# Performance work log

Hardware: AMD Instinct MI355X
Metric: run time of the kernel (lower is better)

## Reference

```python
import jax, jax.numpy as jnp
import numpy as np

N_NODES = 50000
N_EDGES = 800000
HID = 64
N_LAYERS = 3
N_CLASSES = 5
N_GRAPHS = 64
BN_EPS = 1e-5


def setup_inputs() -> dict:
    key = jax.random.key(0)
    ks = jax.random.split(key, 24)
    inp = {}
    inp["x"] = jax.random.normal(ks[0], (N_NODES, 5), dtype=jnp.float32)
    inp["edge_attr"] = jax.random.normal(ks[1], (N_EDGES, 5), dtype=jnp.float32)
    inp["edge_index"] = jax.random.randint(ks[2], (2, N_EDGES), 0, N_NODES, dtype=jnp.int32)
    inp["batch"] = jnp.sort(jax.random.randint(ks[3], (N_NODES,), 0, N_GRAPHS, dtype=jnp.int32))
    s = 0.1
    inp["node_W"] = jax.random.normal(ks[4], (5, HID), dtype=jnp.float32) * s
    inp["node_b"] = jnp.zeros((HID,), jnp.float32)
    inp["edge_W"] = jax.random.normal(ks[5], (5, HID), dtype=jnp.float32) * s
    inp["edge_b"] = jnp.zeros((HID,), jnp.float32)
    # per-layer params stacked on leading dim of size N_LAYERS
    inp["lin_W"] = jax.random.normal(ks[6], (N_LAYERS, HID, HID), dtype=jnp.float32) * s
    inp["lin_b"] = jnp.zeros((N_LAYERS, HID), jnp.float32)
    inp["mlp_W1"] = jax.random.normal(ks[7], (N_LAYERS, HID, HID), dtype=jnp.float32) * s
    inp["mlp_b1"] = jnp.zeros((N_LAYERS, HID), jnp.float32)
    inp["mlp_W2"] = jax.random.normal(ks[8], (N_LAYERS, HID, HID), dtype=jnp.float32) * s
    inp["mlp_b2"] = jnp.zeros((N_LAYERS, HID), jnp.float32)
    inp["bn_g"] = jnp.ones((N_LAYERS, HID), jnp.float32)
    inp["bn_b"] = jnp.zeros((N_LAYERS, HID), jnp.float32)
    inp["head_W1"] = jax.random.normal(ks[9], (HID * 3, HID), dtype=jnp.float32) * s
    inp["head_b1"] = jnp.zeros((HID,), jnp.float32)
    inp["head_W2"] = jax.random.normal(ks[10], (HID, N_CLASSES), dtype=jnp.float32) * s
    inp["head_b2"] = jnp.zeros((N_CLASSES,), jnp.float32)
    return inp


def _forward(x, edge_attr, edge_index, batch, node_W, node_b, edge_W, edge_b,
             lin_W, lin_b, mlp_W1, mlp_b1, mlp_W2, mlp_b2, bn_g, bn_b,
             head_W1, head_b1, head_W2, head_b2):
    h = x @ node_W + node_b                      # [N, H]
    e = edge_attr @ edge_W + edge_b              # [E, H]
    src, dst = edge_index[0], edge_index[1]
    n = h.shape[0]
    inv_std = 1.0 / jnp.sqrt(1.0 + BN_EPS)       # BN eval: running mean=0, var=1
    for l in range(N_LAYERS):
        # GINEConv: m = relu(x_src + Lin(edge_attr)); aggregate sum at dst; eps=0
        m = jax.nn.relu(h[src] + e @ lin_W[l] + lin_b[l])   # [E, H]
        agg = jax.ops.segment_sum(m, dst, num_segments=n)    # [N, H]
        z = h + agg
        z = jax.nn.relu(z @ mlp_W1[l] + mlp_b1[l]) @ mlp_W2[l] + mlp_b2[l]
        z = bn_g[l] * (z * inv_std) + bn_b[l]
        h = jax.nn.relu(z)
    # pooling over graphs
    counts = jax.ops.segment_sum(jnp.ones((n,), h.dtype), batch, num_segments=N_GRAPHS)
    h_sum = jax.ops.segment_sum(h, batch, num_segments=N_GRAPHS)
    h_mean = h_sum / jnp.maximum(counts, 1.0)[:, None]
    h_max = jax.ops.segment_max(h, batch, num_segments=N_GRAPHS)
    h_max = jnp.where(counts[:, None] > 0, h_max, 0.0)
    hc = jnp.concatenate([h_mean, h_max, h_sum], axis=-1)    # [G, 3H]
    return jax.nn.relu(hc @ head_W1 + head_b1) @ head_W2 + head_b2


def reference(x, edge_attr, edge_index, batch, node_W, node_b, edge_W, edge_b,
              lin_W, lin_b, mlp_W1, mlp_b1, mlp_W2, mlp_b2, bn_g, bn_b,
              head_W1, head_b1, head_W2, head_b2):
    return _forward(x, edge_attr, edge_index, batch, node_W, node_b, edge_W, edge_b,
                    lin_W, lin_b, mlp_W1, mlp_b1, mlp_W2, mlp_b2, bn_g, bn_b,
                    head_W1, head_b1, head_W2, head_b2)
```

## Files before the change

kernel.cpp:

```cpp
#include <hip/hip_runtime.h>
#include <hip/hip_bf16.h>

#define HID 64
#define N_LAYERS 3
#define N_GRAPHS 64
#define N_CLASSES 5

__global__ __launch_bounds__(256) void node_embed_kernel(
    const float* __restrict__ x, const float* __restrict__ W,
    const float* __restrict__ b, float* __restrict__ h, int N)
{
    int tid = blockIdx.x * 256 + threadIdx.x;
    int n = tid >> 6;
    int c = tid & 63;
    if (n >= N) return;
    const float* xr = x + (size_t)n * 5;
    float acc = b[c];
#pragma unroll
    for (int k = 0; k < 5; ++k) acc = fmaf(xr[k], W[k * 64 + c], acc);
    h[(size_t)n * 64 + c] = acc;
}

__global__ __launch_bounds__(384) void combine_weights_kernel(
    const float* __restrict__ edge_W, const float* __restrict__ edge_b,
    const float* __restrict__ lin_W, const float* __restrict__ lin_b,
    float* __restrict__ Wc, float* __restrict__ bc)
{
    int l = blockIdx.x;
    int c = threadIdx.x & 63;
    int k = threadIdx.x >> 6;
    const float* LW = lin_W + (size_t)l * 64 * 64;
    if (k < 5) {
        float acc = 0.f;
        for (int j = 0; j < 64; ++j) acc = fmaf(edge_W[k * 64 + j], LW[j * 64 + c], acc);
        Wc[l * 320 + k * 64 + c] = acc;
    } else {
        float acc = lin_b[l * 64 + c];
        for (int j = 0; j < 64; ++j) acc = fmaf(edge_b[j], LW[j * 64 + c], acc);
        bc[l * 64 + c] = acc;
    }
}

__global__ __launch_bounds__(256) void hist_kernel(
    const int* __restrict__ ei, int* __restrict__ deg, int E)
{
    int e = blockIdx.x * 256 + threadIdx.x;
    if (e < E) atomicAdd(&deg[ei[E + e]], 1);
}

__global__ __launch_bounds__(256) void scan1_kernel(
    const int* __restrict__ deg, int* __restrict__ bsum, int N)
{
    __shared__ int s[256];
    int t = threadIdx.x;
    int i = blockIdx.x * 256 + t;
    int v = (i < N) ? deg[i] : 0;
    s[t] = v; __syncthreads();
    for (int off = 128; off > 0; off >>= 1) {
        if (t < off) s[t] += s[t + off];
        __syncthreads();
    }
    if (t == 0) bsum[blockIdx.x] = s[0];
}

__global__ __launch_bounds__(256) void scan2_kernel(
    const int* __restrict__ bsum, int* __restrict__ bpre, int NBLK)
{
    __shared__ int s[256];
    int t = threadIdx.x;
    int v = (t < NBLK) ? bsum[t] : 0;
    s[t] = v; __syncthreads();
    for (int off = 1; off < 256; off <<= 1) {
        int x = (t >= off) ? s[t - off] : 0;
        __syncthreads();
        s[t] += x;
        __syncthreads();
    }
    if (t < NBLK) bpre[t] = s[t] - v;
}

__global__ __launch_bounds__(256) void scan3_kernel(
    const int* __restrict__ deg, const int* __restrict__ bpre,
    int* __restrict__ rowptr, int N, int E)
{
    __shared__ int s[256];
    int t = threadIdx.x;
    int i = blockIdx.x * 256 + t;
    int v = (i < N) ? deg[i] : 0;
    s[t] = v; __syncthreads();
    for (int off = 1; off < 256; off <<= 1) {
        int x = (t >= off) ? s[t - off] : 0;
        __syncthreads();
        s[t] += x;
        __syncthreads();
    }
    if (i < N) rowptr[i] = bpre[blockIdx.x] + s[t] - v;
    if (i == N - 1) rowptr[N] = E;
}

__global__ __launch_bounds__(256) void scatter_kernel(
    const int* __restrict__ ei, const float* __restrict__ ea,
    int* __restrict__ cursor, float* __restrict__ packed,
    int* __restrict__ csrc, int E)
{
    int e = blockIdx.x * 256 + threadIdx.x;
    if (e >= E) return;
    int src = ei[e];
    int dst = ei[E + e];
    int pos = atomicAdd(&cursor[dst], 1);
    const float* p = ea + (size_t)e * 5;
    float4 r0 = make_float4(p[0], p[1], p[2], p[3]);
    float4 r1 = make_float4(p[4], 0.f, 0.f, 0.f);
    float4* q = reinterpret_cast<float4*>(packed + (size_t)pos * 8);
    q[0] = r0;
    q[1] = r1;
    csrc[pos] = src;
}

__global__ __launch_bounds__(256) void agg_kernel(
    const int* __restrict__ rowptr, const int* __restrict__ csrc,
    const float* __restrict__ packed,
    const float* __restrict__ h, const float* __restrict__ Wc,
    const float* __restrict__ bc, float* __restrict__ agg, int N)
{
    int lane = threadIdx.x & 63;
    float w0 = Wc[0 * 64 + lane];
    float w1 = Wc[1 * 64 + lane];
    float w2 = Wc[2 * 64 + lane];
    float w3 = Wc[3 * 64 + lane];
    float w4 = Wc[4 * 64 + lane];
    float bb = bc[lane];

    int wid = (blockIdx.x * 256 + threadIdx.x) >> 6;
    int nw  = (gridDim.x * 256) >> 6;
    for (int n = wid; n < N; n += nw) {
        int eb = rowptr[n];
        int ee = rowptr[n + 1];
        float acc = 0.f;
        for (int base = eb; base < ee; base += 64) {
            int cnt = min(64, ee - base);
            int sv = csrc[base + min(lane, cnt - 1)];
            int j = 0;
            for (; j + 3 < cnt; j += 4) {
                int s0 = __shfl(sv, j + 0);
                int s1 = __shfl(sv, j + 1);
                int s2 = __shfl(sv, j + 2);
                int s3 = __shfl(sv, j + 3);
                float h0 = h[(size_t)s0 * 64 + lane];
                float h1 = h[(size_t)s1 * 64 + lane];
                float h2 = h[(size_t)s2 * 64 + lane];
                float h3 = h[(size_t)s3 * 64 + lane];
                const float4* q = reinterpret_cast<const float4*>(packed + (size_t)(base + j) * 8);
                float4 r0a = q[0], r0b = q[1];
                float4 r1a = q[2], r1b = q[3];
                float4 r2a = q[4], r2b = q[5];
                float4 r3a = q[6], r3b = q[7];
                float m0 = bb + h0;
                m0 = fmaf(r0a.x, w0, m0); m0 = fmaf(r0a.y, w1, m0);
                m0 = fmaf(r0a.z, w2, m0); m0 = fmaf(r0a.w, w3, m0);
                m0 = fmaf(r0b.x, w4, m0);
                float m1 = bb + h1;
                m1 = fmaf(r1a.x, w0, m1); m1 = fmaf(r1a.y, w1, m1);
                m1 = fmaf(r1a.z, w2, m1); m1 = fmaf(r1a.w, w3, m1);
                m1 = fmaf(r1b.x, w4, m1);
                float m2 = bb + h2;
                m2 = fmaf(r2a.x, w0, m2); m2 = fmaf(r2a.y, w1, m2);
                m2 = fmaf(r2a.z, w2, m2); m2 = fmaf(r2a.w, w3, m2);
                m2 = fmaf(r2b.x, w4, m2);
                float m3 = bb + h3;
                m3 = fmaf(r3a.x, w0, m3); m3 = fmaf(r3a.y, w1, m3);
                m3 = fmaf(r3a.z, w2, m3); m3 = fmaf(r3a.w, w3, m3);
                m3 = fmaf(r3b.x, w4, m3);
                acc += fmaxf(m0, 0.f);
                acc += fmaxf(m1, 0.f);
                acc += fmaxf(m2, 0.f);
                acc += fmaxf(m3, 0.f);
            }
            for (; j < cnt; ++j) {
                int s0 = __shfl(sv, j);
                float h0 = h[(size_t)s0 * 64 + lane];
                const float4* q = reinterpret_cast<const float4*>(packed + (size_t)(base + j) * 8);
                float4 r0 = q[0];
                float4 r1 = q[1];
                float m = bb + h0;
                m = fmaf(r0.x, w0, m);
                m = fmaf(r0.y, w1, m);
                m = fmaf(r0.z, w2, m);
                m = fmaf(r0.w, w3, m);
                m = fmaf(r1.x, w4, m);
                acc += fmaxf(m, 0.f);
            }
        }
        agg[(size_t)n * 64 + lane] = acc;
    }
}

__global__ __launch_bounds__(256) void edge_kernel(
    const int* __restrict__ ei, const float* __restrict__ ea,
    const float* __restrict__ h, const float* __restrict__ Wc,
    const float* __restrict__ bc, float* __restrict__ agg, int E)
{
    int lane = threadIdx.x & 63;
    float w0 = Wc[0 * 64 + lane];
    float w1 = Wc[1 * 64 + lane];
    float w2 = Wc[2 * 64 + lane];
    float w3 = Wc[3 * 64 + lane];
    float w4 = Wc[4 * 64 + lane];
    float bb = bc[lane];

    int wave   = (blockIdx.x * 256 + threadIdx.x) >> 6;
    int nwaves = (gridDim.x * 256) >> 6;
    for (int e = wave; e < E; e += nwaves) {
        int src = ei[e];
        int dst = ei[E + e];
        const float* eap = ea + (size_t)e * 5;
        float m = bb + h[(size_t)src * 64 + lane];
        m = fmaf(eap[0], w0, m);
        m = fmaf(eap[1], w1, m);
        m = fmaf(eap[2], w2, m);
        m = fmaf(eap[3], w3, m);
        m = fmaf(eap[4], w4, m);
        m = fmaxf(m, 0.f);
        atomicAdd(&agg[(size_t)dst * 64 + lane], m);
    }
}

__global__ __launch_bounds__(256) void node_mlp_kernel(
    const float* __restrict__ h, const float* __restrict__ agg,
    const float* __restrict__ W1, const float* __restrict__ b1v,
    const float* __restrict__ W2, const float* __restrict__ b2v,
    const float* __restrict__ bng, const float* __restrict__ bnb,
    float* __restrict__ hout, int N)
{
    __shared__ float zbuf[4][64];
    int lane = threadIdx.x & 63;
    int w = threadIdx.x >> 6;

    float w1c[64], w2c[64];
#pragma unroll
    for (int k = 0; k < 64; ++k) w1c[k] = W1[k * 64 + lane];
#pragma unroll
    for (int k = 0; k < 64; ++k) w2c[k] = W2[k * 64 + lane];

    const float inv_std = 0.99999500003749981f;
    float bias1 = b1v[lane];
    float bias2 = b2v[lane];
    float scale = bng[lane] * inv_std;
    float shift = bnb[lane];

    int wid = blockIdx.x * 4 + w;
    int nw  = gridDim.x * 4;
    for (int n = wid; n < N; n += nw) {
        size_t off = (size_t)n * 64 + lane;
        float z = h[off] + agg[off];
        zbuf[w][lane] = z;
        float acc = bias1;
#pragma unroll
        for (int k4 = 0; k4 < 16; ++k4) {
            float4 zk = *reinterpret_cast<const float4*>(&zbuf[w][k4 * 4]);
            acc = fmaf(zk.x, w1c[k4 * 4 + 0], acc);
            acc = fmaf(zk.y, w1c[k4 * 4 + 1], acc);
            acc = fmaf(zk.z, w1c[k4 * 4 + 2], acc);
            acc = fmaf(zk.w, w1c[k4 * 4 + 3], acc);
        }
        float t = fmaxf(acc, 0.f);
        zbuf[w][lane] = t;
        float acc2 = bias2;
#pragma unroll
        for (int k4 = 0; k4 < 16; ++k4) {
            float4 tk = *reinterpret_cast<const float4*>(&zbuf[w][k4 * 4]);
            acc2 = fmaf(tk.x, w2c[k4 * 4 + 0], acc2);
            acc2 = fmaf(tk.y, w2c[k4 * 4 + 1], acc2);
            acc2 = fmaf(tk.z, w2c[k4 * 4 + 2], acc2);
            acc2 = fmaf(tk.w, w2c[k4 * 4 + 3], acc2);
        }
        float y = fmaf(acc2, scale, shift);
        hout[off] = fmaxf(y, 0.f);
    }
}

__global__ __launch_bounds__(256) void pool_kernel(
    const float* __restrict__ h, const int* __restrict__ batch,
    float* __restrict__ psum, int* __restrict__ pmaxi, int* __restrict__ pcount, int N)
{
    int lane = threadIdx.x & 63;
    int chunks = gridDim.x * 4;
    int wid = blockIdx.x * 4 + (threadIdx.x >> 6);
    int CH = (N + chunks - 1) / chunks;
    int n0 = wid * CH;
    int n1 = min(N, n0 + CH);
    if (n0 >= n1) return;

    int gcur = batch[n0];
    float s = 0.f, mx = 0.f;
    int cnt = 0;
    for (int n = n0; n < n1; ++n) {
        int g = batch[n];
        if (g != gcur) {
            atomicAdd(&psum[gcur * 64 + lane], s);
            atomicMax(&pmaxi[gcur * 64 + lane], __float_as_int(mx));
            if (lane == 0) atomicAdd(&pcount[gcur], cnt);
            gcur = g; s = 0.f; mx = 0.f; cnt = 0;
        }
        float v = h[(size_t)n * 64 + lane];
        s += v;
        mx = fmaxf(mx, v);
        ++cnt;
    }
    atomicAdd(&psum[gcur * 64 + lane], s);
    atomicMax(&pmaxi[gcur * 64 + lane], __float_as_int(mx));
    if (lane == 0) atomicAdd(&pcount[gcur], cnt);
}

__global__ __launch_bounds__(256) void head_kernel(
    const float* __restrict__ psum, const int* __restrict__ pmaxi,
    const int* __restrict__ pcount,
    const float* __restrict__ W1, const float* __restrict__ b1,
    const float* __restrict__ W2, const float* __restrict__ b2,
    float* __restrict__ out)
{
    __shared__ float hc[192];
    __shared__ float part[4][64];
    __shared__ float tbuf[64];
    int g = blockIdx.x;
    int tid = threadIdx.x;
    int lane = tid & 63;
    int w = tid >> 6;

    if (tid < 192) {
        int sec = tid >> 6;
        int c = tid & 63;
        float s = psum[g * 64 + c];
        float v;
        if (sec == 0) {
            int cn = pcount[g];
            v = s / fmaxf((float)cn, 1.f);
        } else if (sec == 1) {
            v = __int_as_float(pmaxi[g * 64 + c]);
        } else {
            v = s;
        }
        hc[sec * 64 + c] = v;
    }
    __syncthreads();

    float acc = (w == 0) ? b1[lane] : 0.f;
#pragma unroll
    for (int kk = 0; kk < 48; ++kk) {
        int k = w * 48 + kk;
        acc = fmaf(hc[k], W1[k * 64 + lane], acc);
    }
    part[w][lane] = acc;
    __syncthreads();

    if (w == 0) {
        float t = part[0][lane] + part[1][lane] + part[2][lane] + part[3][lane];
        t = fmaxf(t, 0.f);
        tbuf[lane] = t;
        if (lane < N_CLASSES) {
            float o = b2[lane];
            for (int j = 0; j < 64; ++j) o = fmaf(tbuf[j], W2[j * N_CLASSES + lane], o);
            out[g * N_CLASSES + lane] = o;
        }
    }
}

extern "C" void kernel_launch(void* const* d_in, const int* in_sizes, int n_in,
                              void* d_out, int out_size, void* d_ws, size_t ws_size,
                              hipStream_t stream)
{
    const float* x         = (const float*)d_in[0];
    const float* edge_attr = (const float*)d_in[1];
    const int*   edge_index= (const int*)  d_in[2];
    const int*   batch     = (const int*)  d_in[3];
    const float* node_W    = (const float*)d_in[4];
    const float* node_b    = (const float*)d_in[5];
    const float* edge_W    = (const float*)d_in[6];
    const float* edge_b    = (const float*)d_in[7];
    const float* lin_W     = (const float*)d_in[8];
    const float* lin_b     = (const float*)d_in[9];
    const float* mlp_W1    = (const float*)d_in[10];
    const float* mlp_b1    = (const float*)d_in[11];
    const float* mlp_W2    = (const float*)d_in[12];
    const float* mlp_b2    = (const float*)d_in[13];
    const float* bn_g      = (const float*)d_in[14];
    const float* bn_b      = (const float*)d_in[15];
    const float* head_W1   = (const float*)d_in[16];
    const float* head_b1   = (const float*)d_in[17];
    const float* head_W2   = (const float*)d_in[18];
    const float* head_b2   = (const float*)d_in[19];
    float* out = (float*)d_out;

    const int N = in_sizes[0] / 5;
    const int E = in_sizes[1] / 5;
    const int NBLK = (N + 255) / 256;
    const size_t HB = (size_t)N * HID * sizeof(float);
    const size_t PB = (size_t)E * 8 * sizeof(float);
    const size_t SB = ((size_t)E * sizeof(int) + 1023) & ~(size_t)1023;

    char* ws = (char*)d_ws;
    float* h    = (float*)(ws);
    float* agg  = (float*)(ws + HB);
    const size_t NEEDED = 2 * HB + PB + SB + (size_t)(1 << 20);
    const bool use_csr = (ws_size >= NEEDED);

    char* meta = use_csr ? (ws + 2 * HB + PB + SB) : (ws + 2 * HB);
    float* packed = (float*)(ws + 2 * HB);
    int*   csrc   = (int*)  (ws + 2 * HB + PB);
    int*   rowptr = (int*)(meta);
    int*   cursor = (int*)(meta + 200 * 1024);
    int*   deg    = (int*)(meta + 400 * 1024);
    int*   bsum   = (int*)(meta + 600 * 1024);
    int*   bpre   = (int*)(meta + 601 * 1024);
    float* Wc     = (float*)(meta + 608 * 1024);
    float* bc     = (float*)(meta + 616 * 1024);
    float* psum   = (float*)(meta + 620 * 1024);
    int*   pmaxi  = (int*)(meta + 636 * 1024);
    int*   pcnt   = (int*)(meta + 652 * 1024);

    node_embed_kernel<<<(N * HID + 255) / 256, 256, 0, stream>>>(x, node_W, node_b, h, N);
    combine_weights_kernel<<<N_LAYERS, 384, 0, stream>>>(edge_W, edge_b, lin_W, lin_b, Wc, bc);

    if (use_csr) {
        hipMemsetAsync(deg, 0, (size_t)N * sizeof(int), stream);
        hist_kernel<<<(E + 255) / 256, 256, 0, stream>>>(edge_index, deg, E);
        scan1_kernel<<<NBLK, 256, 0, stream>>>(deg, bsum, N);
        scan2_kernel<<<1, 256, 0, stream>>>(bsum, bpre, NBLK);
        scan3_kernel<<<NBLK, 256, 0, stream>>>(deg, bpre, rowptr, N, E);
        hipMemcpyAsync(cursor, rowptr, (size_t)N * sizeof(int),
                       hipMemcpyDeviceToDevice, stream);
        scatter_kernel<<<(E + 255) / 256, 256, 0, stream>>>(edge_index, edge_attr,
                                                            cursor, packed, csrc, E);
    }

    for (int l = 0; l < N_LAYERS; ++l) {
        if (use_csr) {
            agg_kernel<<<2048, 256, 0, stream>>>(rowptr, csrc, packed, h,
                                                 Wc + l * 320, bc + l * 64, agg, N);
        } else {
            hipMemsetAsync(agg, 0, HB, stream);
            edge_kernel<<<2048, 256, 0, stream>>>(edge_index, edge_attr, h,
                                                  Wc + l * 320, bc + l * 64, agg, E);
        }
        node_mlp_kernel<<<768, 256, 0, stream>>>(h, agg,
                                                 mlp_W1 + (size_t)l * HID * HID, mlp_b1 + l * HID,
                                                 mlp_W2 + (size_t)l * HID * HID, mlp_b2 + l * HID,
                                                 bn_g + l * HID, bn_b + l * HID, h, N);
    }

    hipMemsetAsync(psum, 0, (636 - 620) * 1024 + 16384 + 256, stream);
    pool_kernel<<<196, 256, 0, stream>>>(h, batch, psum, pmaxi, pcnt, N);
    head_kernel<<<N_GRAPHS, 256, 0, stream>>>(psum, pmaxi, pcnt,
                                              head_W1, head_b1, head_W2, head_b2, out);
}
```

Baseline: 444.9 us.

## Build CSR via two-level bucket partition and per-bucket local sort

Replaces the per-node histogram, three-pass scan and global-atomic scatter with a bucket sort. Edges are first grouped into 256-node buckets, staged through shared memory so each chunk writes contiguous runs, then each bucket is sorted locally in shared memory to produce rowptr, csrc and the packed edge attributes. The aim is to cut global atomic contention and random scattered writes during CSR construction. The cost is an extra pass over a temporary record buffer that aliases the h/agg region, plus binary searches in the flush loop. Edge order within a node is no longer deterministic.

```diff
diff --git a/kernel.cpp b/kernel.cpp
--- a/kernel.cpp
+++ b/kernel.cpp
@@ -5,6 +5,8 @@
 #define N_LAYERS 3
 #define N_GRAPHS 64
 #define N_CLASSES 5
+#define CHUNK 4096
+#define MAXB 1024
 
 __global__ __launch_bounds__(256) void node_embed_kernel(
     const float* __restrict__ x, const float* __restrict__ W,
@@ -41,80 +43,142 @@
     }
 }
 
-__global__ __launch_bounds__(256) void hist_kernel(
-    const int* __restrict__ ei, int* __restrict__ deg, int E)
-{
-    int e = blockIdx.x * 256 + threadIdx.x;
-    if (e < E) atomicAdd(&deg[ei[E + e]], 1);
-}
-
-__global__ __launch_bounds__(256) void scan1_kernel(
-    const int* __restrict__ deg, int* __restrict__ bsum, int N)
-{
-    __shared__ int s[256];
+
+__global__ __launch_bounds__(256) void bucket_hist_kernel(
+    const int* __restrict__ ei, int* __restrict__ bhist, int E, int nb)
+{
+    __shared__ int lh[MAXB];
+    for (int i = threadIdx.x; i < nb; i += 256) lh[i] = 0;
+    __syncthreads();
+    int stride = gridDim.x * 256;
+    for (int e = blockIdx.x * 256 + threadIdx.x; e < E; e += stride)
+        atomicAdd(&lh[ei[E + e] >> 8], 1);
+    __syncthreads();
+    for (int i = threadIdx.x; i < nb; i += 256)
+        if (lh[i]) atomicAdd(&bhist[i], lh[i]);
+}
+
+__global__ __launch_bounds__(1024) void bucket_scan_kernel(
+    const int* __restrict__ bhist, int* __restrict__ boff, int* __restrict__ bcur,
+    int nb, int E)
+{
+    __shared__ int s[MAXB];
     int t = threadIdx.x;
-    int i = blockIdx.x * 256 + t;
-    int v = (i < N) ? deg[i] : 0;
+    int v = (t < nb) ? bhist[t] : 0;
     s[t] = v; __syncthreads();
-    for (int off = 128; off > 0; off >>= 1) {
-        if (t < off) s[t] += s[t + off];
-        __syncthreads();
-    }
-    if (t == 0) bsum[blockIdx.x] = s[0];
-}
-
-__global__ __launch_bounds__(256) void scan2_kernel(
-    const int* __restrict__ bsum, int* __restrict__ bpre, int NBLK)
-{
-    __shared__ int s[256];
-    int t = threadIdx.x;
-    int v = (t < NBLK) ? bsum[t] : 0;
-    s[t] = v; __syncthreads();
-    for (int off = 1; off < 256; off <<= 1) {
+    for (int off = 1; off < MAXB; off <<= 1) {
         int x = (t >= off) ? s[t - off] : 0;
         __syncthreads();
         s[t] += x;
         __syncthreads();
     }
-    if (t < NBLK) bpre[t] = s[t] - v;
-}
-
-__global__ __launch_bounds__(256) void scan3_kernel(
-    const int* __restrict__ deg, const int* __restrict__ bpre,
-    int* __restrict__ rowptr, int N, int E)
-{
-    __shared__ int s[256];
+    if (t < nb) { int ex = s[t] - v; boff[t] = ex; bcur[t] = ex; }
+    if (t == 0) boff[nb] = E;
+}
+
+__global__ __launch_bounds__(1024) void partition_kernel(
+    const int* __restrict__ ei, const float* __restrict__ ea,
+    int* __restrict__ bcur, float* __restrict__ tmprec, int E, int nb)
+{
+    __shared__ float stage[CHUNK * 8];
+    __shared__ int ihist[MAXB];
+    __shared__ int iscan[MAXB];
+    __shared__ int cnt2[MAXB];
+    __shared__ int gbase[MAXB];
     int t = threadIdx.x;
-    int i = blockIdx.x * 256 + t;
-    int v = (i < N) ? deg[i] : 0;
-    s[t] = v; __syncthreads();
+    int e0 = blockIdx.x * CHUNK;
+    int cnt = min(CHUNK, E - e0);
+
+    ihist[t] = 0;
+    cnt2[t] = 0;
+    __syncthreads();
+    for (int i = t; i < cnt; i += 1024)
+        atomicAdd(&ihist[ei[E + e0 + i] >> 8], 1);
+    __syncthreads();
+    int v = ihist[t];
+    iscan[t] = v; __syncthreads();
+    for (int off = 1; off < MAXB; off <<= 1) {
+        int x = (t >= off) ? iscan[t - off] : 0;
+        __syncthreads();
+        iscan[t] += x;
+        __syncthreads();
+    }
+    iscan[t] -= v;
+    gbase[t] = v ? atomicAdd(&bcur[t], v) : 0;
+    __syncthreads();
+    for (int i = t; i < cnt; i += 1024) {
+        int e = e0 + i;
+        int src = ei[e];
+        int dst = ei[E + e];
+        const float* p = ea + (size_t)e * 5;
+        int b = dst >> 8;
+        int r = atomicAdd(&cnt2[b], 1);
+        int slot = iscan[b] + r;
+        float4* q = reinterpret_cast<float4*>(stage + (size_t)slot * 8);
+        q[0] = make_float4(__int_as_float(src), __int_as_float(dst), p[0], p[1]);
+        q[1] = make_float4(p[2], p[3], p[4], 0.f);
+    }
+    __syncthreads();
+    for (int slot = t; slot < cnt; slot += 1024) {
+        int lo = 0, hi = MAXB - 1;
+        while (lo < hi) {
+            int mid = (lo + hi + 1) >> 1;
+            if (iscan[mid] <= slot) lo = mid; else hi = mid - 1;
+        }
+        int b = lo;
+        size_t g = (size_t)gbase[b] + (size_t)(slot - iscan[b]);
+        const float4* q = reinterpret_cast<const float4*>(stage + (size_t)slot * 8);
+        float4 r0 = q[0], r1 = q[1];
+        float4* o = reinterpret_cast<float4*>(tmprec + g * 8);
+        o[0] = r0;
+        o[1] = r1;
+    }
+}
+
+__global__ __launch_bounds__(256) void bucket_sort_kernel(
+    const int* __restrict__ boff, const float* __restrict__ tmprec,
+    int* __restrict__ rowptr, int* __restrict__ csrc, float* __restrict__ packed,
+    int N, int E, int nb)
+{
+    __shared__ int cnt[256];
+    __shared__ int loff[256];
+    int g = blockIdx.x;
+    int t = threadIdx.x;
+    int s0 = boff[g], s1 = boff[g + 1];
+    int nb0 = g << 8;
+    cnt[t] = 0;
+    __syncthreads();
+    for (int i = s0 + t; i < s1; i += 256) {
+        int dst = __float_as_int(tmprec[(size_t)i * 8 + 1]);
+        atomicAdd(&cnt[dst & 255], 1);
+    }
+    __syncthreads();
+    int v = cnt[t];
+    loff[t] = v; __syncthreads();
     for (int off = 1; off < 256; off <<= 1) {
-        int x = (t >= off) ? s[t - off] : 0;
+        int x = (t >= off) ? loff[t - off] : 0;
         __syncthreads();
-        s[t] += x;
+        loff[t] += x;
         __syncthreads();
     }
-    if (i < N) rowptr[i] = bpre[blockIdx.x] + s[t] - v;
-    if (i == N - 1) rowptr[N] = E;
-}
-
-__global__ __launch_bounds__(256) void scatter_kernel(
-    const int* __restrict__ ei, const float* __restrict__ ea,
-    int* __restrict__ cursor, float* __restrict__ packed,
-    int* __restrict__ csrc, int E)
-{
-    int e = blockIdx.x * 256 + threadIdx.x;
-    if (e >= E) return;
-    int src = ei[e];
-    int dst = ei[E + e];
-    int pos = atomicAdd(&cursor[dst], 1);
-    const float* p = ea + (size_t)e * 5;
-    float4 r0 = make_float4(p[0], p[1], p[2], p[3]);
-    float4 r1 = make_float4(p[4], 0.f, 0.f, 0.f);
-    float4* q = reinterpret_cast<float4*>(packed + (size_t)pos * 8);
-    q[0] = r0;
-    q[1] = r1;
-    csrc[pos] = src;
+    loff[t] -= v;
+    __syncthreads();
+    if (nb0 + t < N) rowptr[nb0 + t] = s0 + loff[t];
+    if (g == nb - 1 && t == 0) rowptr[N] = E;
+    cnt[t] = 0;
+    __syncthreads();
+    for (int i = s0 + t; i < s1; i += 256) {
+        const float4* q = reinterpret_cast<const float4*>(tmprec + (size_t)i * 8);
+        float4 r0 = q[0], r1 = q[1];
+        int src = __float_as_int(r0.x);
+        int d = __float_as_int(r0.y) & 255;
+        int r = atomicAdd(&cnt[d], 1);
+        size_t pos = (size_t)s0 + (size_t)loff[d] + (size_t)r;
+        csrc[pos] = src;
+        float4* o = reinterpret_cast<float4*>(packed + pos * 8);
+        o[0] = make_float4(r0.z, r0.w, r1.x, r1.y);
+        o[1] = make_float4(r1.z, 0.f, 0.f, 0.f);
+    }
 }
 
 __global__ __launch_bounds__(256) void agg_kernel(
@@ -391,47 +455,50 @@
     const float* head_b2   = (const float*)d_in[19];
     float* out = (float*)d_out;
 
-    const int N = in_sizes[0] / 5;
-    const int E = in_sizes[1] / 5;
-    const int NBLK = (N + 255) / 256;
-    const size_t HB = (size_t)N * HID * sizeof(float);
-    const size_t PB = (size_t)E * 8 * sizeof(float);
-    const size_t SB = ((size_t)E * sizeof(int) + 1023) & ~(size_t)1023;
+    const int N  = in_sizes[0] / 5;
+    const int E  = in_sizes[1] / 5;
+    const int nb = (N + 255) >> 8;
+
+    const size_t HB  = (size_t)N * HID * sizeof(float);
+    const size_t PB  = (size_t)E * 8 * sizeof(float);
+    const size_t TR  = (size_t)E * 8 * sizeof(float);
+    size_t R0 = (2 * HB > TR) ? 2 * HB : TR;
+    R0 = (R0 + 4095) & ~(size_t)4095;
+    const size_t SBc = (((size_t)E * sizeof(int)) + 1023) & ~(size_t)1023;
 
     char* ws = (char*)d_ws;
-    float* h    = (float*)(ws);
-    float* agg  = (float*)(ws + HB);
-    const size_t NEEDED = 2 * HB + PB + SB + (size_t)(1 << 20);
-    const bool use_csr = (ws_size >= NEEDED);
-
-    char* meta = use_csr ? (ws + 2 * HB + PB + SB) : (ws + 2 * HB);
-    float* packed = (float*)(ws + 2 * HB);
-    int*   csrc   = (int*)  (ws + 2 * HB + PB);
+    float* h      = (float*)(ws);
+    float* agg    = (float*)(ws + HB);
+    float* tmprec = (float*)(ws);
+    float* packed = (float*)(ws + R0);
+    int*   csrc   = (int*)  (ws + R0 + PB);
+    char*  meta   = ws + R0 + PB + SBc;
     int*   rowptr = (int*)(meta);
-    int*   cursor = (int*)(meta + 200 * 1024);
-    int*   deg    = (int*)(meta + 400 * 1024);
-    int*   bsum   = (int*)(meta + 600 * 1024);
-    int*   bpre   = (int*)(meta + 601 * 1024);
-    float* Wc     = (float*)(meta + 608 * 1024);
-    float* bc     = (float*)(meta + 616 * 1024);
-    float* psum   = (float*)(meta + 620 * 1024);
-    int*   pmaxi  = (int*)(meta + 636 * 1024);
-    int*   pcnt   = (int*)(meta + 652 * 1024);
+    int*   boff   = (int*)(meta + 200 * 1024);
+    int*   bcur   = (int*)(meta + 208 * 1024);
+    int*   bhist  = (int*)(meta + 212 * 1024);
+    float* Wc     = (float*)(meta + 216 * 1024);
+    float* bc     = (float*)(meta + 224 * 1024);
+    float* psum   = (float*)(meta + 228 * 1024);
+    int*   pmaxi  = (int*)(meta + 244 * 1024);
+    int*   pcnt   = (int*)(meta + 260 * 1024);
+
+    const size_t NEEDED = R0 + PB + SBc + 264 * 1024 + (1 << 20);
+    const bool use_csr = (ws_size >= NEEDED) && (nb <= MAXB);
+
+    combine_weights_kernel<<<N_LAYERS, 384, 0, stream>>>(edge_W, edge_b, lin_W, lin_b, Wc, bc);
+
+    if (use_csr) {
+        hipMemsetAsync(bhist, 0, (size_t)nb * sizeof(int), stream);
+        bucket_hist_kernel<<<256, 256, 0, stream>>>(edge_index, bhist, E, nb);
+        bucket_scan_kernel<<<1, 1024, 0, stream>>>(bhist, boff, bcur, nb, E);
+        partition_kernel<<<(E + CHUNK - 1) / CHUNK, 1024, 0, stream>>>(
+            edge_index, edge_attr, bcur, tmprec, E, nb);
+        bucket_sort_kernel<<<nb, 256, 0, stream>>>(boff, tmprec, rowptr, csrc,
+                                                   packed, N, E, nb);
+    }
 
     node_embed_kernel<<<(N * HID + 255) / 256, 256, 0, stream>>>(x, node_W, node_b, h, N);
-    combine_weights_kernel<<<N_LAYERS, 384, 0, stream>>>(edge_W, edge_b, lin_W, lin_b, Wc, bc);
-
-    if (use_csr) {
-        hipMemsetAsync(deg, 0, (size_t)N * sizeof(int), stream);
-        hist_kernel<<<(E + 255) / 256, 256, 0, stream>>>(edge_index, deg, E);
-        scan1_kernel<<<NBLK, 256, 0, stream>>>(deg, bsum, N);
-        scan2_kernel<<<1, 256, 0, stream>>>(bsum, bpre, NBLK);
-        scan3_kernel<<<NBLK, 256, 0, stream>>>(deg, bpre, rowptr, N, E);
-        hipMemcpyAsync(cursor, rowptr, (size_t)N * sizeof(int),
-                       hipMemcpyDeviceToDevice, stream);
-        scatter_kernel<<<(E + 255) / 256, 256, 0, stream>>>(edge_index, edge_attr,
-                                                            cursor, packed, csrc, E);
-    }
 
     for (int l = 0; l < N_LAYERS; ++l) {
         if (use_csr) {
@@ -448,7 +515,7 @@
                                                  bn_g + l * HID, bn_b + l * HID, h, N);
     }
 
-    hipMemsetAsync(psum, 0, (636 - 620) * 1024 + 16384 + 256, stream);
+    hipMemsetAsync(psum, 0, 16 * 1024 + 16 * 1024 + 256, stream);
     pool_kernel<<<196, 256, 0, stream>>>(h, batch, psum, pmaxi, pcnt, N);
     head_kernel<<<N_GRAPHS, 256, 0, stream>>>(psum, pmaxi, pcnt,
                                               head_W1, head_b1, head_W2, head_b2, out);
```

After: 400.6 us. 10.0% less time.
